# Kernel tuning notes

Measured on AMD Instinct MI355X. Metric: run time of the kernel, lower is better.

The kernel has to match this reference:

```python
import jax, jax.numpy as jnp
import numpy as np

NUM_EXPERTS = 8
TOP_K = 2
D = 512
F = 2048
B, L = 4, 1024


def setup_inputs() -> dict:
    key = jax.random.key(0)
    ks = jax.random.split(key, 5)
    std = D ** -0.5
    return {
        "x": jax.random.normal(ks[0], (B, L, D), jnp.float32),
        "gate_w": jax.random.normal(ks[1], (NUM_EXPERTS, D), jnp.float32) * std,
        "w1": jax.random.normal(ks[2], (NUM_EXPERTS, F, D), jnp.float32) * std,
        "w2": jax.random.normal(ks[3], (NUM_EXPERTS, D, F), jnp.float32) * (F ** -0.5),
        "w3": jax.random.normal(ks[4], (NUM_EXPERTS, F, D), jnp.float32) * std,
    }


def reference(x, gate_w, w1, w2, w3):
    b, l, d = x.shape
    xf = x.reshape(-1, d)                      # [T, D]
    T = xf.shape[0]
    router_logits = xf @ gate_w.T              # [T, E]
    # top-k routing in float32 (as in original), softmax over selected logits
    topk_w, topk_idx = jax.lax.top_k(router_logits.astype(jnp.float32), TOP_K)
    topk_w = jax.nn.softmax(topk_w, axis=-1).astype(x.dtype)  # [T, K]
    # combine weights per (token, expert): scatter top-k weights into dense [T, E]
    cw = jnp.zeros((T, NUM_EXPERTS), x.dtype)
    cw = cw.at[jnp.arange(T)[:, None], topk_idx].add(topk_w)
    # per-expert gated FFN (SiLU(x w1^T) * (x w3^T)) w2^T, batched over experts
    h = jax.nn.silu(jnp.einsum('td,efd->etf', xf, w1)) * jnp.einsum('td,efd->etf', xf, w3)
    y = jnp.einsum('etf,edf->etd', h, w2)      # [E, T, D]
    out = jnp.einsum('te,etd->td', cw, y)      # weighted combine
    return out.reshape(b, l, d), router_logits
```

## Files before the change

kernel.cpp:

```cpp
#include <hip/hip_runtime.h>

#define TTOK 4096
#define NEXP 8
#define DDIM 512
#define FDIM 2048
#define HROWS 8576

typedef __attribute__((ext_vector_type(8))) short short8;
typedef __attribute__((ext_vector_type(4))) float floatx4;

#define BAR()  __builtin_amdgcn_s_barrier()
#define SBAR() __builtin_amdgcn_sched_barrier(0)

__device__ __forceinline__ ushort f2b(float f) {
  unsigned u = __float_as_uint(f);
  u += 0x7fffu + ((u >> 16) & 1u);
  return (ushort)(u >> 16);
}

__device__ __forceinline__ void load16(void* lds, const void* g) {
  __builtin_amdgcn_global_load_lds(
      (const __attribute__((address_space(1))) unsigned int*)g,
      (__attribute__((address_space(3))) unsigned int*)lds, 16, 0, 0);
}


__global__ __launch_bounds__(256) void k_front(
    const float* __restrict__ x, const float* __restrict__ gw,
    float* __restrict__ logits, int* __restrict__ tok_e,
    float2* __restrict__ tok_w, float* __restrict__ outz,
    ushort* __restrict__ xb,
    const float* __restrict__ w1, ushort* __restrict__ w1t,
    const float* __restrict__ w3, ushort* __restrict__ w3t)
{
  __shared__ ushort sm[4096];
  const int tid = threadIdx.x;
  if (blockIdx.x < TTOK / 4) {
    float4 zz = {0.f, 0.f, 0.f, 0.f};
    float4* orow = (float4*)(outz + (size_t)blockIdx.x * 4 * DDIM);
    orow[tid] = zz;
    orow[tid + 256] = zz;
    const int lane = tid & 63;
    const int t = blockIdx.x * 4 + (tid >> 6);
    float xv[8];
#pragma unroll
    for (int i = 0; i < 8; ++i) xv[i] = x[(size_t)t * DDIM + lane + 64 * i];
#pragma unroll
    for (int i = 0; i < 8; ++i) xb[(size_t)t * DDIM + lane + 64 * i] = f2b(xv[i]);
    float lg[8];
#pragma unroll
    for (int e = 0; e < 8; ++e) {
      float a = 0.f;
#pragma unroll
      for (int i = 0; i < 8; ++i) a += xv[i] * gw[e * DDIM + lane + 64 * i];
#pragma unroll
      for (int s = 32; s; s >>= 1) a += __shfl_xor(a, s, 64);
      lg[e] = a;
    }
    if (lane < 8) logits[(size_t)t * 8 + lane] = lg[lane];
    if (lane == 0) {
      int i0 = 0; float v0 = lg[0];
#pragma unroll
      for (int e = 1; e < 8; ++e) { if (lg[e] > v0) { v0 = lg[e]; i0 = e; } }
      int i1 = -1; float v1 = -3.4e38f;
#pragma unroll
      for (int e = 0; e < 8; ++e) { if (e != i0 && lg[e] > v1) { v1 = lg[e]; i1 = e; } }
      float ex = expf(v1 - v0);
      float inv = 1.f / (1.f + ex);
      tok_e[t] = i0 | (i1 << 4);
      tok_w[t] = make_float2(inv, ex * inv);
    }
    return;
  }
  int bid = blockIdx.x - TTOK / 4;
  const float* src = (bid < 2048) ? w1 : w3;
  ushort* dst = (bid < 2048) ? w1t : w3t;
  if (bid >= 2048) bid -= 2048;
  const int r0 = (bid >> 2) * 32;
  const int c0 = (bid & 3) * 128;
#pragma unroll
  for (int i = 0; i < 4; ++i) {
    int j = i * 1024 + tid * 4;
    int lr = j >> 7, lc = j & 127;
    float4 v = *(const float4*)&src[(size_t)(r0 + lr) * 512 + c0 + lc];
    ushort4 b = { f2b(v.x), f2b(v.y), f2b(v.z), f2b(v.w) };
    int ord = (lr >> 4) * 4 + (lc >> 5);
    int slot = (lr & 15) + 16 * ((lc >> 3) & 3);
    *(ushort4*)&sm[(ord * 64 + slot) * 8 + (lc & 7)] = b;
  }
  __syncthreads();
  const size_t tb0 = ((size_t)(r0 >> 4) * 16 + (c0 >> 5)) * 512;
#pragma unroll
  for (int rt = 0; rt < 2; ++rt)
    *(short8*)&dst[tb0 + (size_t)rt * 16 * 512 + tid * 8] =
        *(const short8*)&sm[rt * 2048 + tid * 8];
}

__global__ __launch_bounds__(1024) void k_build(
    const int* __restrict__ tok_e, const float2* __restrict__ tok_w,
    int* __restrict__ counts, int* __restrict__ lists, float* __restrict__ wts)
{
  const int e = blockIdx.x;
  const int tid = threadIdx.x;
  const int lane = tid & 63, wid = tid >> 6;
  __shared__ int wcnt[16];
  __shared__ int sbase;
  if (tid == 0) sbase = 0;
  __syncthreads();

  for (int c = 0; c < TTOK; c += 1024) {
    int t = c + tid;
    int pe = tok_e[t];
    bool m0 = (pe & 15) == e;
    bool m1 = ((pe >> 4) & 15) == e;
    bool m = m0 || m1;
    unsigned long long b = __ballot(m);
    int lpre = __popcll(b & ((1ull << lane) - 1ull));
    if (lane == 0) wcnt[wid] = __popcll(b);
    __syncthreads();
    int woff = 0;
#pragma unroll
    for (int i = 0; i < 16; ++i) if (i < wid) woff += wcnt[i];
    if (m) {
      float2 w = tok_w[t];
      int pos = sbase + woff + lpre;
      lists[e * TTOK + pos] = t;
      wts[e * TTOK + pos] = m0 ? w.x : w.y;
    }
    __syncthreads();
    if (tid == 0) {
      int s = 0;
#pragma unroll
      for (int i = 0; i < 16; ++i) s += wcnt[i];
      sbase += s;
    }
    __syncthreads();
  }
  if (tid == 0) counts[e] = sbase;
}

__global__ __launch_bounds__(256) void k_gather(
    const ushort* __restrict__ xb, const int* __restrict__ counts,
    const int* __restrict__ lists, ushort* __restrict__ Xg)
{
  int pp[9];
  pp[0] = 0;
#pragma unroll
  for (int i = 0; i < 8; ++i) pp[i + 1] = pp[i] + ((counts[i] + 31) & ~31);
  int gid = blockIdx.x * 256 + threadIdx.x;
  int gr = gid >> 6, dg = gid & 63;
  if (gr >= pp[8]) return;
  int e = 0;
  while (e < 7 && gr >= pp[e + 1]) ++e;
  int p = gr - pp[e];
  size_t dst = ((size_t)(gr >> 4) * 16 + (dg >> 2)) * 512
             + ((gr & 15) + 16 * (dg & 3)) * 8;
  short8 o = (short8)0;
  if (p < counts[e]) {
    int t = lists[e * TTOK + p];
    o = *(const short8*)&xb[(size_t)t * DDIM + dg * 8];
  }
  *(short8*)&Xg[dst] = o;
}

__global__ __launch_bounds__(512) void k_ffn1(
    const ushort* __restrict__ Xg, const ushort* __restrict__ w1t,
    const ushort* __restrict__ w3t, const int* __restrict__ counts,
    ushort* __restrict__ H,
    const float* __restrict__ w2, ushort* __restrict__ w2t)
{
  __shared__ ushort smem[36864];
  const int tid = threadIdx.x;

  const int grp = blockIdx.x >> 3, lane8 = blockIdx.x & 7;
  const int q3 = grp % 3, gq = grp / 3;

  if (q3 == 2) {
    int bid = gq * 8 + lane8;
    ushort* sm = smem;
    const int r0 = (bid >> 4) * 32;
    const int c0 = (bid & 15) * 128;
#pragma unroll
    for (int i = 0; i < 2; ++i) {
      int j = i * 2048 + tid * 4;
      int lr = j >> 7, lc = j & 127;
      float4 v = *(const float4*)&w2[(size_t)(r0 + lr) * 2048 + c0 + lc];
      ushort4 b = { f2b(v.x), f2b(v.y), f2b(v.z), f2b(v.w) };
      int ord = (lr >> 4) * 4 + (lc >> 5);
      int slot = (lr & 15) + 16 * ((lc >> 3) & 3);
      *(ushort4*)&sm[(ord * 64 + slot) * 8 + (lc & 7)] = b;
    }
    __syncthreads();
    const size_t tb0 = ((size_t)(r0 >> 4) * 64 + (c0 >> 5)) * 512;
    int rt = tid >> 8, s = tid & 255;
    *(short8*)&w2t[tb0 + (size_t)rt * 64 * 512 + s * 8] =
        *(const short8*)&sm[rt * 2048 + s * 8];
    return;
  }

  const int gemmid = (gq * 2 + q3) * 8 + lane8;
  const int widx = (gemmid & 7) * 512 + (gemmid >> 3);
  const int mt = widx & 31, e = (widx >> 5) & 7, ft = widx >> 8;
  const int ne = counts[e];
  const int m0 = mt * 128;
  if (m0 >= ne) return;
  const int f0 = ft * 128;
  int hb = 0;
#pragma unroll
  for (int i = 0; i < 7; ++i) if (i < e) hb += (counts[i] + 31) & ~31;
  const int wid = tid >> 6, lane = tid & 63;
  const int wm = wid >> 2, wn = wid & 3;
  const int lr = lane & 15, lgp = lane >> 4;

  const int rtX0 = (hb + m0) >> 4;
  const ushort* sx = Xg  + ((size_t)(rtX0 + wid) * 16) * 512 + lane * 8;
  const ushort* s1 = w1t + ((size_t)(e * 128 + (f0 >> 4) + wid) * 16) * 512 + lane * 8;
  const ushort* s3 = w3t + ((size_t)(e * 128 + (f0 >> 4) + wid) * 16) * 512 + lane * 8;

#define FFN1_STAGE(B)                                                       \
  { char* base = (char*)smem + (B) * 24576 + wid * 1024;                    \
    load16(base, sx);                                                       \
    load16(base + 8192, s1);                                                \
    load16(base + 16384, s3);                                               \
    sx += 512; s1 += 512; s3 += 512; }

#define FFN1_COMPUTE(B)                                                     \
  { const ushort* cb = smem + (B) * 12288;                                  \
    short8 af[4], b1[2], b3[2];                                             \
    _Pragma("unroll")                                                       \
    for (int mf = 0; mf < 4; ++mf)                                          \
      af[mf] = *(const short8*)&cb[(wm * 4 + mf) * 512 + lane * 8];         \
    _Pragma("unroll")                                                       \
    for (int nf = 0; nf < 2; ++nf) {                                        \
      b1[nf] = *(const short8*)&cb[4096 + (wn * 2 + nf) * 512 + lane * 8];  \
      b3[nf] = *(const short8*)&cb[8192 + (wn * 2 + nf) * 512 + lane * 8];  \
    }                                                                       \
    _Pragma("unroll")                                                       \
    for (int mf = 0; mf < 4; ++mf)                                          \
      _Pragma("unroll")                                                     \
      for (int nf = 0; nf < 2; ++nf) {                                      \
        acc1[mf][nf] = __builtin_amdgcn_mfma_f32_16x16x32_bf16(             \
            af[mf], b1[nf], acc1[mf][nf], 0, 0, 0);                         \
        acc3[mf][nf] = __builtin_amdgcn_mfma_f32_16x16x32_bf16(             \
            af[mf], b3[nf], acc3[mf][nf], 0, 0, 0);                         \
      } }

  floatx4 acc1[4][2], acc3[4][2];
#pragma unroll
  for (int a = 0; a < 4; ++a)
#pragma unroll
    for (int b = 0; b < 2; ++b) { acc1[a][b] = (floatx4)0.f; acc3[a][b] = (floatx4)0.f; }

  FFN1_STAGE(0);
  FFN1_STAGE(1);
#pragma unroll
  for (int t = 0; t < 16; ++t) {
    if (t + 2 < 16) FFN1_STAGE((t + 2) % 3);
    if (t < 14)      asm volatile("s_waitcnt vmcnt(6)" ::: "memory");
    else if (t < 15) asm volatile("s_waitcnt vmcnt(3)" ::: "memory");
    else             asm volatile("s_waitcnt vmcnt(0)" ::: "memory");
    BAR(); SBAR();
    FFN1_COMPUTE(t % 3);
    SBAR(); BAR();
  }

  __syncthreads();
  ushort* hstage = smem;
#pragma unroll
  for (int mf = 0; mf < 4; ++mf) {
#pragma unroll
    for (int nf = 0; nf < 2; ++nf) {
      const int tloc = (wm * 4 + mf) * 4 + wn;
      const int slotc = (nf * 2 + (lr >> 3)) & 3;
      const int bidx = tloc * 512 + slotc * 128 + (lr & 7);
      floatx4 v1 = acc1[mf][nf], v3 = acc3[mf][nf];
#pragma unroll
      for (int j = 0; j < 4; ++j) {
        float h1 = v1[j], h3 = v3[j];
        float sig = 1.f / (1.f + __expf(-h1));
        hstage[bidx + (lgp * 4 + j) * 8] = f2b(h1 * sig * h3);
      }
    }
  }
  __syncthreads();
  const int ktBase = f0 >> 5;
#pragma unroll
  for (int i = 0; i < 4; ++i) {
    int s = i * 512 + tid;
    int tloc = s >> 6, off = s & 63;
    int rt_l = tloc >> 2, kt_l = tloc & 3;
    if (m0 + rt_l * 16 + (off & 15) < ne)
      *(short8*)&H[((size_t)(rtX0 + rt_l) * 64 + ktBase + kt_l) * 512 + off * 8] =
          *(const short8*)&hstage[s * 8];
  }
#undef FFN1_STAGE
#undef FFN1_COMPUTE
}

__global__ __launch_bounds__(512) void k_ffn2(
    const ushort* __restrict__ Ht, const ushort* __restrict__ w2t,
    const int* __restrict__ counts, const int* __restrict__ lists,
    const float* __restrict__ wts, float* __restrict__ out)
{
  const int bid = blockIdx.x;
  const int widx = (bid & 7) * 256 + (bid >> 3);
  const int mt = widx & 31, e = (widx >> 5) & 7;
  const int rest = widx >> 8;
  const int dt = rest & 3, ks = rest >> 2;
  const int ne = counts[e];
  const int m0 = mt * 128;
  if (m0 >= ne) return;
  const int d0 = dt * 128;
  int hb = 0;
#pragma unroll
  for (int i = 0; i < 7; ++i) if (i < e) hb += (counts[i] + 31) & ~31;
  const int tid = threadIdx.x;
  const int wid = tid >> 6, lane = tid & 63;
  const int wm = wid >> 2, wn = wid & 3;
  const int lr = lane & 15, lgp = lane >> 4;

  __shared__ ushort Hls[2][8192], W2ls[2][8192];
  __shared__ int toks[128];
  __shared__ float twt[128];

  if (tid < 128) {
    int p = m0 + tid;
    bool v = p < ne;
    toks[tid] = v ? lists[e * TTOK + p] : 0;
    twt[tid] = v ? wts[e * TTOK + p] : 0.f;
  }

  const int rtH0 = (hb + m0) >> 4;
  const int kb = ks * 32;
  const ushort* sh = Ht  + ((size_t)(rtH0 + wid) * 64 + kb) * 512 + lane * 8;
  const ushort* sw = w2t + ((size_t)(e * 32 + (d0 >> 4) + wid) * 64 + kb) * 512 + lane * 8;

#define FFN2_STAGE(B)                                                      \
  { load16((char*)&Hls[B][0]  + (wid * 2) * 1024, sh);                     \
    load16((char*)&Hls[B][0]  + (wid * 2 + 1) * 1024, sh + 512);           \
    load16((char*)&W2ls[B][0] + (wid * 2) * 1024, sw);                     \
    load16((char*)&W2ls[B][0] + (wid * 2 + 1) * 1024, sw + 512);           \
    sh += 1024; sw += 1024; }

#define FFN2_COMPUTE(B)                                                    \
  { _Pragma("unroll")                                                      \
    for (int kk = 0; kk < 2; ++kk) {                                       \
      short8 af[4], bf[2];                                                 \
      _Pragma("unroll")                                                    \
      for (int mf = 0; mf < 4; ++mf)                                       \
        af[mf] = *(const short8*)&Hls[B][((wm * 4 + mf) * 2 + kk) * 512 + lane * 8]; \
      _Pragma("unroll")                                                    \
      for (int nf = 0; nf < 2; ++nf)                                       \
        bf[nf] = *(const short8*)&W2ls[B][((wn * 2 + nf) * 2 + kk) * 512 + lane * 8]; \
      _Pragma("unroll")                                                    \
      for (int mf = 0; mf < 4; ++mf)                                       \
        _Pragma("unroll")                                                  \
        for (int nf = 0; nf < 2; ++nf)                                     \
          acc[mf][nf] = __builtin_amdgcn_mfma_f32_16x16x32_bf16(           \
              af[mf], bf[nf], acc[mf][nf], 0, 0, 0);                       \
    } }

  floatx4 acc[4][2];
#pragma unroll
  for (int a = 0; a < 4; ++a)
#pragma unroll
    for (int b = 0; b < 2; ++b) acc[a][b] = (floatx4)0.f;

  FFN2_STAGE(0);
  for (int t = 0; t < 16; t += 2) {
    FFN2_STAGE(1);
    asm volatile("s_waitcnt vmcnt(4)" ::: "memory");
    BAR(); SBAR();
    FFN2_COMPUTE(0);
    SBAR(); BAR();
    if (t + 2 < 16) {
      FFN2_STAGE(0);
      asm volatile("s_waitcnt vmcnt(4)" ::: "memory");
    } else {
      asm volatile("s_waitcnt vmcnt(0)" ::: "memory");
    }
    BAR(); SBAR();
    FFN2_COMPUTE(1);
    SBAR(); BAR();
  }

#pragma unroll
  for (int mf = 0; mf < 4; ++mf) {
#pragma unroll
    for (int j = 0; j < 4; ++j) {
      int rloc = wm * 64 + mf * 16 + lgp * 4 + j;
      int p = m0 + rloc;
      if (p < ne) {
        int t = toks[rloc];
        float w = twt[rloc];
#pragma unroll
        for (int nf = 0; nf < 2; ++nf) {
          int d = d0 + wn * 32 + nf * 16 + lr;
          atomicAdd(&out[(size_t)t * DDIM + d], w * acc[mf][nf][j]);
        }
      }
    }
  }
#undef FFN2_STAGE
#undef FFN2_COMPUTE
}

extern "C" void kernel_launch(void* const* d_in, const int* in_sizes, int n_in,
                              void* d_out, int out_size, void* d_ws, size_t ws_size,
                              hipStream_t stream) {
  const float* x  = (const float*)d_in[0];
  const float* gw = (const float*)d_in[1];
  const float* w1 = (const float*)d_in[2];
  const float* w2 = (const float*)d_in[3];
  const float* w3 = (const float*)d_in[4];
  float* out = (float*)d_out;
  float* logits = out + (size_t)TTOK * DDIM;

  int* counts = (int*)d_ws;
  int* tok_e  = counts + 16;
  float2* tok_w = (float2*)(tok_e + TTOK);
  int* lists  = (int*)(tok_w + TTOK);
  float* wts  = (float*)(lists + NEXP * TTOK);
  ushort* xb  = (ushort*)(wts + NEXP * TTOK);
  ushort* w1t = xb + (size_t)TTOK * DDIM;
  ushort* w3t = w1t + (size_t)NEXP * FDIM * DDIM;
  ushort* w2t = w3t + (size_t)NEXP * FDIM * DDIM;
  ushort* Xg  = w2t + (size_t)NEXP * DDIM * FDIM;
  ushort* H   = Xg + (size_t)HROWS * DDIM;

  k_front<<<TTOK / 4 + 4096, 256, 0, stream>>>(x, gw, logits, tok_e, tok_w,
                                               out, xb, w1, w1t, w3, w3t);
  k_build<<<NEXP, 1024, 0, stream>>>(tok_e, tok_w, counts, lists, wts);
  k_gather<<<(8448 * 64) / 256, 256, 0, stream>>>(xb, counts, lists, Xg);

  k_ffn1<<<4096 + 2048, 512, 0, stream>>>(Xg, w1t, w3t, counts, H, w2, w2t);
  k_ffn2<<<2048, 512, 0, stream>>>(H, w2t, counts, lists, wts, out);
}
```

Before: 138.5 us.

## Fuse token gather into FFN1 by loading rows directly via routing lists

Removes the separate gather kernel that built a permuted, tiled copy of the bf16 activations per expert. FFN1 now loads the token indices for its 128-row tile into shared memory and issues direct-to-LDS loads from the original activation rows using those indices. This saves one kernel launch and the write/read of the gathered buffer, at the cost of less coalesced row-indexed global loads and an extra barrier per tile. Padding rows reuse the first token of the expert list instead of zeros.

```diff
diff --git a/kernel.cpp b/kernel.cpp
--- a/kernel.cpp
+++ b/kernel.cpp
@@ -139,37 +139,14 @@
   if (tid == 0) counts[e] = sbase;
 }
 
-__global__ __launch_bounds__(256) void k_gather(
-    const ushort* __restrict__ xb, const int* __restrict__ counts,
-    const int* __restrict__ lists, ushort* __restrict__ Xg)
-{
-  int pp[9];
-  pp[0] = 0;
-#pragma unroll
-  for (int i = 0; i < 8; ++i) pp[i + 1] = pp[i] + ((counts[i] + 31) & ~31);
-  int gid = blockIdx.x * 256 + threadIdx.x;
-  int gr = gid >> 6, dg = gid & 63;
-  if (gr >= pp[8]) return;
-  int e = 0;
-  while (e < 7 && gr >= pp[e + 1]) ++e;
-  int p = gr - pp[e];
-  size_t dst = ((size_t)(gr >> 4) * 16 + (dg >> 2)) * 512
-             + ((gr & 15) + 16 * (dg & 3)) * 8;
-  short8 o = (short8)0;
-  if (p < counts[e]) {
-    int t = lists[e * TTOK + p];
-    o = *(const short8*)&xb[(size_t)t * DDIM + dg * 8];
-  }
-  *(short8*)&Xg[dst] = o;
-}
-
 __global__ __launch_bounds__(512) void k_ffn1(
-    const ushort* __restrict__ Xg, const ushort* __restrict__ w1t,
+    const ushort* __restrict__ xb, const ushort* __restrict__ w1t,
     const ushort* __restrict__ w3t, const int* __restrict__ counts,
-    ushort* __restrict__ H,
+    const int* __restrict__ lists, ushort* __restrict__ H,
     const float* __restrict__ w2, ushort* __restrict__ w2t)
 {
   __shared__ ushort smem[36864];
+  __shared__ int toksL[128];
   const int tid = threadIdx.x;
 
   const int grp = blockIdx.x >> 3, lane8 = blockIdx.x & 7;
@@ -212,8 +189,14 @@
   const int wm = wid >> 2, wn = wid & 3;
   const int lr = lane & 15, lgp = lane >> 4;
 
+  if (tid < 128) {
+    int p = m0 + tid;
+    toksL[tid] = (p < ne) ? lists[e * TTOK + p] : lists[e * TTOK];
+  }
+  __syncthreads();
+
   const int rtX0 = (hb + m0) >> 4;
-  const ushort* sx = Xg  + ((size_t)(rtX0 + wid) * 16) * 512 + lane * 8;
+  const ushort* sx = xb + (size_t)toksL[wid * 16 + lr] * DDIM + lgp * 8;
   const ushort* s1 = w1t + ((size_t)(e * 128 + (f0 >> 4) + wid) * 16) * 512 + lane * 8;
   const ushort* s3 = w3t + ((size_t)(e * 128 + (f0 >> 4) + wid) * 16) * 512 + lane * 8;
 
@@ -222,7 +205,7 @@
     load16(base, sx);                                                       \
     load16(base + 8192, s1);                                                \
     load16(base + 16384, s3);                                               \
-    sx += 512; s1 += 512; s3 += 512; }
+    sx += 32; s1 += 512; s3 += 512; }
 
 #define FFN1_COMPUTE(B)                                                     \
   { const ushort* cb = smem + (B) * 12288;                                  \
@@ -425,14 +408,12 @@
   ushort* w1t = xb + (size_t)TTOK * DDIM;
   ushort* w3t = w1t + (size_t)NEXP * FDIM * DDIM;
   ushort* w2t = w3t + (size_t)NEXP * FDIM * DDIM;
-  ushort* Xg  = w2t + (size_t)NEXP * DDIM * FDIM;
-  ushort* H   = Xg + (size_t)HROWS * DDIM;
+  ushort* H   = w2t + (size_t)NEXP * DDIM * FDIM;
 
   k_front<<<TTOK / 4 + 4096, 256, 0, stream>>>(x, gw, logits, tok_e, tok_w,
                                                out, xb, w1, w1t, w3, w3t);
   k_build<<<NEXP, 1024, 0, stream>>>(tok_e, tok_w, counts, lists, wts);
-  k_gather<<<(8448 * 64) / 256, 256, 0, stream>>>(xb, counts, lists, Xg);
-
-  k_ffn1<<<4096 + 2048, 512, 0, stream>>>(Xg, w1t, w3t, counts, H, w2, w2t);
+
+  k_ffn1<<<4096 + 2048, 512, 0, stream>>>(xb, w1t, w3t, counts, lists, H, w2, w2t);
   k_ffn2<<<2048, 512, 0, stream>>>(H, w2t, counts, lists, wts, out);
 }
```

Result: no change. 136.8 us (-1.2%).
